# Kernel optimization log

Hardware: AMD Instinct MI355X
Metric: run time of the kernel (lower is better)

Reference implementation:

```python
import jax, jax.numpy as jnp
import numpy as np

HIDDEN = 1024
HEADS = 16
HEAD_DIM = HIDDEN // HEADS


def setup_inputs() -> dict:
    key = jax.random.key(0)
    ks = jax.random.split(key, 8)
    B, S = 2, 2048
    scale = 1.0 / np.sqrt(HIDDEN)
    inp = {
        "hidden_states": jax.random.normal(ks[0], (B, S, HIDDEN), dtype=jnp.float32),
        "attention_mask": jnp.zeros((B, 1, 1, S), dtype=jnp.float32),
        "q_w": jax.random.normal(ks[1], (HIDDEN, HIDDEN), dtype=jnp.float32) * scale,
        "q_b": jnp.zeros((HIDDEN,), dtype=jnp.float32),
        "k_w": jax.random.normal(ks[2], (HIDDEN, HIDDEN), dtype=jnp.float32) * scale,
        "k_b": jnp.zeros((HIDDEN,), dtype=jnp.float32),
        "v_w": jax.random.normal(ks[3], (HIDDEN, HIDDEN), dtype=jnp.float32) * scale,
        "v_b": jnp.zeros((HIDDEN,), dtype=jnp.float32),
    }
    return inp


def _split_heads(x):
    # [B, S, H] -> [B, heads, S, head_dim]
    B, S, _ = x.shape
    return x.reshape(B, S, HEADS, HEAD_DIM).transpose(0, 2, 1, 3)


def reference(hidden_states, attention_mask, q_w, q_b, k_w, k_b, v_w, v_b):
    # Linear projections (torch Linear: x @ W.T + b; here weights stored as [in, out])
    q = _split_heads(hidden_states @ q_w + q_b)  # [B, h, S, d]
    k = _split_heads(hidden_states @ k_w + k_b)
    v = _split_heads(hidden_states @ v_w + v_b)

    scores = jnp.einsum("bhqd,bhkd->bhqk", q, k) / jnp.sqrt(jnp.float32(HEAD_DIM))
    scores = scores + attention_mask  # additive mask, broadcast [B,1,1,S]
    probs = jax.nn.softmax(scores, axis=-1)
    # dropout prob = 0.0 -> identity
    ctx = jnp.einsum("bhqk,bhkd->bhqd", probs, v)  # [B, h, S, d]
    B, _, S, _ = ctx.shape
    ctx = ctx.transpose(0, 2, 1, 3).reshape(B, S, HIDDEN)
    return ctx
```

## Files before the change

kernel.cpp:

```cpp
#include <hip/hip_runtime.h>

typedef __bf16 bf16;
typedef __attribute__((ext_vector_type(8))) __bf16 bf16x8;
typedef __attribute__((ext_vector_type(4))) __bf16 bf16x4;
typedef __attribute__((ext_vector_type(4))) float f32x4;

#define MFMA(a, b, c) __builtin_amdgcn_mfma_f32_16x16x32_bf16((a), (b), (c), 0, 0, 0)
#define LOG2E 1.44269504088896340736f

__device__ __forceinline__ bf16x8 cvt8(float4 a, float4 b) {
  bf16x8 r;
  r[0] = (bf16)a.x; r[1] = (bf16)a.y; r[2] = (bf16)a.z; r[3] = (bf16)a.w;
  r[4] = (bf16)b.x; r[5] = (bf16)b.y; r[6] = (bf16)b.z; r[7] = (bf16)b.w;
  return r;
}

__device__ __forceinline__ void stage16(const bf16* g, bf16* l) {
  __builtin_amdgcn_global_load_lds(
      (const __attribute__((address_space(1))) void*)g,
      (__attribute__((address_space(3))) void*)l, 16, 0, 0);
}

__global__ __launch_bounds__(256)
void cvt(const float* __restrict__ hs, const float* __restrict__ qw,
         const float* __restrict__ kw, const float* __restrict__ vw,
         bf16* __restrict__ Xb, bf16* __restrict__ Wt) {
  const int bid = blockIdx.x, tid = threadIdx.x;
  if (bid < 2048) {
    size_t off = (size_t)bid * 2048 + tid * 8;
    float4 x0 = *(const float4*)(hs + off);
    float4 x1 = *(const float4*)(hs + off + 4);
    *(bf16x8*)(Xb + off) = cvt8(x0, x1);
  } else {
    int t = bid - 2048;
    int z = t >> 8, ti = t & 255;
    const float* W = (z == 0) ? qw : (z == 1) ? kw : vw;
    int k0 = (ti >> 4) * 64, n0 = (ti & 15) * 64;
    __shared__ bf16 T[64 * 72];
    #pragma unroll
    for (int i = 0; i < 16; ++i) {
      int e = i * 256 + tid;
      int kr = e >> 6, nc = e & 63;
      T[nc * 72 + kr] = (bf16)W[(size_t)(k0 + kr) * 1024 + n0 + nc];
    }
    __syncthreads();
    #pragma unroll
    for (int i = 0; i < 2; ++i) {
      int e = i * 256 + tid;
      int nr = e >> 3, kg = e & 7;
      *(bf16x8*)(Wt + (size_t)z * 1048576 + (size_t)(n0 + nr) * 1024 + k0 + kg * 8) =
          *(const bf16x8*)&T[nr * 72 + kg * 8];
    }
  }
}

__global__ __launch_bounds__(256, 3)
void qkv_gemm(const bf16* __restrict__ Xb, const bf16* __restrict__ Wt,
              const float* __restrict__ qbias, const float* __restrict__ kbias,
              const float* __restrict__ vbias,
              bf16* __restrict__ qo, bf16* __restrict__ ko, bf16* __restrict__ vo) {
  const int blk = blockIdx.x;
  const int xcd = blk & 7, slot = blk >> 3;
  const int mb = xcd * 4 + slot / 24;
  const int nb = slot % 24;
  const int z = nb >> 3, nbm = nb & 7;
  const bf16* W = Wt + (size_t)z * 1048576;

  const int tid = threadIdx.x;
  const int wave = tid >> 6, lane = tid & 63, quad = lane >> 4, c = lane & 15;
  const int wr = wave >> 1, wc = wave & 1;
  const int lrow = lane >> 3;
  const int lg = (lane & 7) ^ lrow;

  __shared__ bf16 As[128 * 64];
  __shared__ bf16 Bs[128 * 64];

  f32x4 acc[4][4] = {};

  for (int k0 = 0; k0 < 1024; k0 += 64) {
    #pragma unroll
    for (int i = 0; i < 4; ++i) {
      int r = wave * 32 + i * 8;
      stage16(Xb + (size_t)(mb * 128 + r + lrow) * 1024 + k0 + lg * 8, &As[r * 64]);
      stage16(W + (size_t)(nbm * 128 + r + lrow) * 1024 + k0 + lg * 8, &Bs[r * 64]);
    }
    __syncthreads();
    #pragma unroll
    for (int ch = 0; ch < 2; ++ch) {
      bf16x8 af[4];
      #pragma unroll
      for (int rt = 0; rt < 4; ++rt) {
        int row = wr * 64 + rt * 16 + c;
        af[rt] = *(const bf16x8*)&As[row * 64 + ((((ch << 2) | quad) ^ (c & 7)) << 3)];
      }
      #pragma unroll
      for (int nt = 0; nt < 4; ++nt) {
        int row = wc * 64 + nt * 16 + c;
        bf16x8 bfrag = *(const bf16x8*)&Bs[row * 64 + ((((ch << 2) | quad) ^ (c & 7)) << 3)];
        #pragma unroll
        for (int rt = 0; rt < 4; ++rt)
          acc[rt][nt] = MFMA(af[rt], bfrag, acc[rt][nt]);
      }
    }
    __syncthreads();
  }

  const float* bias = (z == 0) ? qbias : (z == 1) ? kbias : vbias;
  float bv[4];
  #pragma unroll
  for (int nt = 0; nt < 4; ++nt)
    bv[nt] = bias[nbm * 128 + wc * 64 + nt * 16 + c];

  if (z == 2) {
    #pragma unroll
    for (int rt = 0; rt < 4; ++rt)
      #pragma unroll
      for (int nt = 0; nt < 4; ++nt) {
        int m0 = mb * 128 + wr * 64 + rt * 16 + 4 * quad;
        int n = nbm * 128 + wc * 64 + nt * 16 + c;
        bf16x4 pk;
        #pragma unroll
        for (int reg = 0; reg < 4; ++reg) pk[reg] = (bf16)(acc[rt][nt][reg] + bv[nt]);
        int b = m0 >> 11, s0 = m0 & 2047, h = n >> 6, d = n & 63;
        *(bf16x4*)&vo[(((size_t)b * 16 + h) * 64 + d) * 2048 + s0] = pk;
      }
  } else {
    bf16* dst = (z == 0) ? qo : ko;
    const float scale = (z == 0) ? 0.125f * LOG2E : 1.0f;
    #pragma unroll
    for (int rt = 0; rt < 4; ++rt)
      #pragma unroll
      for (int nt = 0; nt < 4; ++nt)
        #pragma unroll
        for (int reg = 0; reg < 4; ++reg) {
          float v = (acc[rt][nt][reg] + bv[nt]) * scale;
          int m = mb * 128 + wr * 64 + rt * 16 + 4 * quad + reg;
          int n = nbm * 128 + wc * 64 + nt * 16 + c;
          int b = m >> 11, s = m & 2047, h = n >> 6, d = n & 63;
          dst[(((size_t)b * 16 + h) * 2048 + s) * 64 + d] = (bf16)v;
        }
  }
}

__global__ __launch_bounds__(512, 4)
void attn(const bf16* __restrict__ qg, const bf16* __restrict__ kg,
          const bf16* __restrict__ vtg, const float* __restrict__ mask,
          float* __restrict__ out) {
  const int blk = blockIdx.x;
  const int xcd = blk & 7, slot = blk >> 3;
  const int bh = xcd * 4 + (slot >> 4);
  const int qblk = slot & 15;
  const int b = bh >> 4, h = bh & 15;
  const int tid = threadIdx.x;
  const int wave = tid >> 6, lane = tid & 63, quad = lane >> 4, c = lane & 15;
  const int lrow = lane >> 3, lg = (lane & 7) ^ lrow;

  __shared__ bf16 Ks[64 * 64];
  __shared__ bf16 Vs[64 * 64];
  __shared__ bf16 Ps[8][1024];

  const bf16* qb_ = qg + (size_t)bh * 2048 * 64;
  const bf16* kb_ = kg + (size_t)bh * 2048 * 64;
  const bf16* vb_ = vtg + (size_t)bh * 64 * 2048;

  bf16x8 qf[2];
  #pragma unroll
  for (int ch = 0; ch < 2; ++ch)
    qf[ch] = *(const bf16x8*)(qb_ +
        (size_t)(qblk * 128 + wave * 16 + c) * 64 + ch * 32 + quad * 8);

  f32x4 o[4] = {};
  float lsum[4] = {};

  for (int kt = 0; kt < 32; ++kt) {
    {
      int r = wave * 8;
      stage16(kb_ + (size_t)(kt * 64 + r + lrow) * 64 + lg * 8, &Ks[r * 64]);
      stage16(vb_ + (size_t)(r + lrow) * 2048 + kt * 64 + lg * 8, &Vs[r * 64]);
    }
    __syncthreads();

    f32x4 s[4] = {};
    #pragma unroll
    for (int nt = 0; nt < 4; ++nt)
      #pragma unroll
      for (int ch = 0; ch < 2; ++ch) {
        bf16x8 kf = *(const bf16x8*)&Ks[(nt * 16 + c) * 64 +
                                        ((((ch << 2) | quad) ^ (c & 7)) << 3)];
        s[nt] = MFMA(qf[ch], kf, s[nt]);
      }

    float mv[4];
    #pragma unroll
    for (int nt = 0; nt < 4; ++nt)
      mv[nt] = mask[b * 2048 + kt * 64 + nt * 16 + c] * LOG2E;

    #pragma unroll
    for (int nt = 0; nt < 4; ++nt)
      #pragma unroll
      for (int reg = 0; reg < 4; ++reg) {
        float p = __builtin_amdgcn_exp2f(s[nt][reg] + mv[nt]);
        lsum[reg] += p;
        int r = 4 * quad + reg;
        int gk = nt * 2 + (c >> 3);
        Ps[wave][r * 64 + ((gk ^ (r & 7)) << 3) + (c & 7)] = (bf16)p;
      }
    __asm__ volatile("s_waitcnt lgkmcnt(0)" ::: "memory");

    #pragma unroll
    for (int ch = 0; ch < 2; ++ch) {
      bf16x8 pa = *(const bf16x8*)&Ps[wave][c * 64 +
                                           ((((ch << 2) | quad) ^ (c & 7)) << 3)];
      #pragma unroll
      for (int nt = 0; nt < 4; ++nt) {
        bf16x8 vf = *(const bf16x8*)&Vs[(nt * 16 + c) * 64 +
                                        ((((ch << 2) | quad) ^ (c & 7)) << 3)];
        o[nt] = MFMA(pa, vf, o[nt]);
      }
    }
    __syncthreads();
  }

  #pragma unroll
  for (int reg = 0; reg < 4; ++reg) {
    float l = lsum[reg];
    #pragma unroll
    for (int off = 1; off < 16; off <<= 1) l += __shfl_xor(l, off, 64);
    float inv = 1.0f / l;
    int srow = qblk * 128 + wave * 16 + 4 * quad + reg;
    #pragma unroll
    for (int nt = 0; nt < 4; ++nt)
      out[((size_t)b * 2048 + srow) * 1024 + h * 64 + nt * 16 + c] =
          o[nt][reg] * inv;
  }
}

extern "C" void kernel_launch(void* const* d_in, const int* in_sizes, int n_in,
                              void* d_out, int out_size, void* d_ws, size_t ws_size,
                              hipStream_t stream) {
  const float* hs   = (const float*)d_in[0];
  const float* mask = (const float*)d_in[1];
  const float* qw   = (const float*)d_in[2];
  const float* qb   = (const float*)d_in[3];
  const float* kw   = (const float*)d_in[4];
  const float* kb   = (const float*)d_in[5];
  const float* vw   = (const float*)d_in[6];
  const float* vb   = (const float*)d_in[7];
  float* out = (float*)d_out;

  bf16* Xb   = (bf16*)d_ws;
  bf16* Wt   = Xb + (size_t)4096 * 1024;
  bf16* q_ws = Wt + (size_t)3 * 1048576;
  bf16* k_ws = q_ws + (size_t)4096 * 1024;
  bf16* v_ws = k_ws + (size_t)4096 * 1024;

  cvt<<<dim3(2816), 256, 0, stream>>>(hs, qw, kw, vw, Xb, Wt);
  qkv_gemm<<<dim3(768), 256, 0, stream>>>(Xb, Wt, qb, kb, vb, q_ws, k_ws, v_ws);
  attn<<<dim3(512), 512, 0, stream>>>(q_ws, k_ws, v_ws, mask, out);
}
```

Baseline: 178.6 us.

## Double-buffer K/V tiles, keep P in registers via bpermute, shrink GEMM K-step

The attention kernel now double-buffers the K and V tiles in LDS, prefetching tile kt+1 while computing tile kt, so one barrier per iteration replaces two. It computes S transposed (K as the A operand) and redistributes the packed bf16 probabilities across lanes with ds_bpermute instead of writing them to and reading them from a per-wave LDS buffer. The row sum becomes one scalar per lane, reduced with fewer shuffles. The QKV GEMM switches to a 32-wide K step with precomputed addresses and a 4-way swizzle, halving LDS use, and the attention kernel drops its occupancy hint. Risks are more barriers in the GEMM, since it now has twice as many K iterations, and the cost of the permutes.

```diff
diff --git a/kernel.cpp b/kernel.cpp
--- a/kernel.cpp
+++ b/kernel.cpp
@@ -3,6 +3,7 @@
 typedef __bf16 bf16;
 typedef __attribute__((ext_vector_type(8))) __bf16 bf16x8;
 typedef __attribute__((ext_vector_type(4))) __bf16 bf16x4;
+typedef __attribute__((ext_vector_type(2))) __bf16 bf16x2;
 typedef __attribute__((ext_vector_type(4))) float f32x4;
 
 #define MFMA(a, b, c) __builtin_amdgcn_mfma_f32_16x16x32_bf16((a), (b), (c), 0, 0, 0)
@@ -13,6 +14,12 @@
   r[0] = (bf16)a.x; r[1] = (bf16)a.y; r[2] = (bf16)a.z; r[3] = (bf16)a.w;
   r[4] = (bf16)b.x; r[5] = (bf16)b.y; r[6] = (bf16)b.z; r[7] = (bf16)b.w;
   return r;
+}
+
+__device__ __forceinline__ int pk2(float x, float y) {
+  union { bf16x2 h; int i; } u;
+  u.h[0] = (bf16)x; u.h[1] = (bf16)y;
+  return u.i;
 }
 
 __device__ __forceinline__ void stage16(const bf16* g, bf16* l) {
@@ -69,38 +76,45 @@
   const int tid = threadIdx.x;
   const int wave = tid >> 6, lane = tid & 63, quad = lane >> 4, c = lane & 15;
   const int wr = wave >> 1, wc = wave & 1;
-  const int lrow = lane >> 3;
-  const int lg = (lane & 7) ^ lrow;
-
-  __shared__ bf16 As[128 * 64];
-  __shared__ bf16 Bs[128 * 64];
+  const int r4 = lane >> 2;
+  const int g4 = (lane & 3) ^ (r4 & 3);
+
+  __shared__ bf16 As[128 * 32];
+  __shared__ bf16 Bs[128 * 32];
+
+  const bf16* aS0 = Xb + (size_t)(mb * 128 + wave * 16 + r4) * 1024 + g4 * 8;
+  const bf16* aS1 = aS0 + (size_t)64 * 1024;
+  const bf16* bS0 = W + (size_t)(nbm * 128 + wave * 16 + r4) * 1024 + g4 * 8;
+  const bf16* bS1 = bS0 + (size_t)64 * 1024;
+  bf16* aD0 = &As[(wave * 16) * 32];
+  bf16* aD1 = &As[(64 + wave * 16) * 32];
+  bf16* bD0 = &Bs[(wave * 16) * 32];
+  bf16* bD1 = &Bs[(64 + wave * 16) * 32];
+
+  int aOff[4], bOff[4];
+  #pragma unroll
+  for (int t = 0; t < 4; ++t) {
+    aOff[t] = (wr * 64 + t * 16 + c) * 32 + ((quad ^ (c & 3)) << 3);
+    bOff[t] = (wc * 64 + t * 16 + c) * 32 + ((quad ^ (c & 3)) << 3);
+  }
 
   f32x4 acc[4][4] = {};
 
-  for (int k0 = 0; k0 < 1024; k0 += 64) {
-    #pragma unroll
-    for (int i = 0; i < 4; ++i) {
-      int r = wave * 32 + i * 8;
-      stage16(Xb + (size_t)(mb * 128 + r + lrow) * 1024 + k0 + lg * 8, &As[r * 64]);
-      stage16(W + (size_t)(nbm * 128 + r + lrow) * 1024 + k0 + lg * 8, &Bs[r * 64]);
-    }
-    __syncthreads();
-    #pragma unroll
-    for (int ch = 0; ch < 2; ++ch) {
-      bf16x8 af[4];
-      #pragma unroll
-      for (int rt = 0; rt < 4; ++rt) {
-        int row = wr * 64 + rt * 16 + c;
-        af[rt] = *(const bf16x8*)&As[row * 64 + ((((ch << 2) | quad) ^ (c & 7)) << 3)];
-      }
-      #pragma unroll
-      for (int nt = 0; nt < 4; ++nt) {
-        int row = wc * 64 + nt * 16 + c;
-        bf16x8 bfrag = *(const bf16x8*)&Bs[row * 64 + ((((ch << 2) | quad) ^ (c & 7)) << 3)];
-        #pragma unroll
-        for (int rt = 0; rt < 4; ++rt)
-          acc[rt][nt] = MFMA(af[rt], bfrag, acc[rt][nt]);
-      }
+  for (int k0 = 0; k0 < 1024; k0 += 32) {
+    stage16(aS0 + k0, aD0);
+    stage16(aS1 + k0, aD1);
+    stage16(bS0 + k0, bD0);
+    stage16(bS1 + k0, bD1);
+    __syncthreads();
+    bf16x8 af[4];
+    #pragma unroll
+    for (int rt = 0; rt < 4; ++rt) af[rt] = *(const bf16x8*)&As[aOff[rt]];
+    #pragma unroll
+    for (int nt = 0; nt < 4; ++nt) {
+      bf16x8 bfrag = *(const bf16x8*)&Bs[bOff[nt]];
+      #pragma unroll
+      for (int rt = 0; rt < 4; ++rt)
+        acc[rt][nt] = MFMA(af[rt], bfrag, acc[rt][nt]);
     }
     __syncthreads();
   }
@@ -142,7 +156,7 @@
   }
 }
 
-__global__ __launch_bounds__(512, 4)
+__global__ __launch_bounds__(512)
 void attn(const bf16* __restrict__ qg, const bf16* __restrict__ kg,
           const bf16* __restrict__ vtg, const float* __restrict__ mask,
           float* __restrict__ out) {
@@ -155,13 +169,13 @@
   const int wave = tid >> 6, lane = tid & 63, quad = lane >> 4, c = lane & 15;
   const int lrow = lane >> 3, lg = (lane & 7) ^ lrow;
 
-  __shared__ bf16 Ks[64 * 64];
-  __shared__ bf16 Vs[64 * 64];
-  __shared__ bf16 Ps[8][1024];
+  __shared__ bf16 Ks[2][64 * 64];
+  __shared__ bf16 Vs[2][64 * 64];
 
   const bf16* qb_ = qg + (size_t)bh * 2048 * 64;
   const bf16* kb_ = kg + (size_t)bh * 2048 * 64;
   const bf16* vb_ = vtg + (size_t)bh * 64 * 2048;
+  const float* mk_ = mask + (size_t)b * 2048;
 
   bf16x8 qf[2];
   #pragma unroll
@@ -169,64 +183,86 @@
     qf[ch] = *(const bf16x8*)(qb_ +
         (size_t)(qblk * 128 + wave * 16 + c) * 64 + ch * 32 + quad * 8);
 
+  const int idx0 = ((2 * (quad & 1) + (quad >> 1)) * 16 + c) << 2;
+  const int idx1 = idx0 ^ 64;
+  const bool qhi = (quad >= 2);
+  const bool qodd = (quad & 1);
+
   f32x4 o[4] = {};
-  float lsum[4] = {};
+  float lsum = 0.f;
+
+  {
+    int r = wave * 8;
+    stage16(kb_ + (size_t)(r + lrow) * 64 + lg * 8, &Ks[0][r * 64]);
+    stage16(vb_ + (size_t)(r + lrow) * 2048 + lg * 8, &Vs[0][r * 64]);
+  }
 
   for (int kt = 0; kt < 32; ++kt) {
-    {
+    __syncthreads();
+    const int cur = kt & 1;
+    if (kt < 31) {
       int r = wave * 8;
-      stage16(kb_ + (size_t)(kt * 64 + r + lrow) * 64 + lg * 8, &Ks[r * 64]);
-      stage16(vb_ + (size_t)(r + lrow) * 2048 + kt * 64 + lg * 8, &Vs[r * 64]);
-    }
-    __syncthreads();
+      stage16(kb_ + (size_t)((kt + 1) * 64 + r + lrow) * 64 + lg * 8,
+              &Ks[cur ^ 1][r * 64]);
+      stage16(vb_ + (size_t)(r + lrow) * 2048 + (kt + 1) * 64 + lg * 8,
+              &Vs[cur ^ 1][r * 64]);
+    }
 
     f32x4 s[4] = {};
     #pragma unroll
     for (int nt = 0; nt < 4; ++nt)
       #pragma unroll
       for (int ch = 0; ch < 2; ++ch) {
-        bf16x8 kf = *(const bf16x8*)&Ks[(nt * 16 + c) * 64 +
-                                        ((((ch << 2) | quad) ^ (c & 7)) << 3)];
-        s[nt] = MFMA(qf[ch], kf, s[nt]);
-      }
-
-    float mv[4];
-    #pragma unroll
-    for (int nt = 0; nt < 4; ++nt)
-      mv[nt] = mask[b * 2048 + kt * 64 + nt * 16 + c] * LOG2E;
-
-    #pragma unroll
-    for (int nt = 0; nt < 4; ++nt)
+        bf16x8 kf = *(const bf16x8*)&Ks[cur][(nt * 16 + c) * 64 +
+                                            ((((ch << 2) | quad) ^ (c & 7)) << 3)];
+        s[nt] = MFMA(kf, qf[ch], s[nt]);
+      }
+
+    int pk[4][2];
+    #pragma unroll
+    for (int nt = 0; nt < 4; ++nt) {
+      float4 mv = *(const float4*)&mk_[kt * 64 + nt * 16 + 4 * quad];
+      float mvf[4] = {mv.x, mv.y, mv.z, mv.w};
+      float p[4];
       #pragma unroll
       for (int reg = 0; reg < 4; ++reg) {
-        float p = __builtin_amdgcn_exp2f(s[nt][reg] + mv[nt]);
-        lsum[reg] += p;
-        int r = 4 * quad + reg;
-        int gk = nt * 2 + (c >> 3);
-        Ps[wave][r * 64 + ((gk ^ (r & 7)) << 3) + (c & 7)] = (bf16)p;
-      }
-    __asm__ volatile("s_waitcnt lgkmcnt(0)" ::: "memory");
+        p[reg] = __builtin_amdgcn_exp2f(fmaf(mvf[reg], LOG2E, s[nt][reg]));
+        lsum += p[reg];
+      }
+      pk[nt][0] = pk2(p[0], p[1]);
+      pk[nt][1] = pk2(p[2], p[3]);
+    }
 
     #pragma unroll
     for (int ch = 0; ch < 2; ++ch) {
-      bf16x8 pa = *(const bf16x8*)&Ps[wave][c * 64 +
-                                           ((((ch << 2) | quad) ^ (c & 7)) << 3)];
+      const int tA = 2 * ch, tB = 2 * ch + 1;
+      int sA0 = qodd ? pk[tB][0] : pk[tA][0];
+      int sA1 = qodd ? pk[tB][1] : pk[tA][1];
+      int sB0 = qodd ? pk[tA][0] : pk[tB][0];
+      int sB1 = qodd ? pk[tA][1] : pk[tB][1];
+      int rA0 = __builtin_amdgcn_ds_bpermute(idx0, sA0);
+      int rA1 = __builtin_amdgcn_ds_bpermute(idx0, sA1);
+      int rB0 = __builtin_amdgcn_ds_bpermute(idx1, sB0);
+      int rB1 = __builtin_amdgcn_ds_bpermute(idx1, sB1);
+      union { int i[4]; bf16x8 v; } pa;
+      pa.i[0] = qhi ? rB0 : rA0;
+      pa.i[1] = qhi ? rB1 : rA1;
+      pa.i[2] = qhi ? rA0 : rB0;
+      pa.i[3] = qhi ? rA1 : rB1;
       #pragma unroll
       for (int nt = 0; nt < 4; ++nt) {
-        bf16x8 vf = *(const bf16x8*)&Vs[(nt * 16 + c) * 64 +
-                                        ((((ch << 2) | quad) ^ (c & 7)) << 3)];
-        o[nt] = MFMA(pa, vf, o[nt]);
-      }
-    }
-    __syncthreads();
-  }
-
+        bf16x8 vf = *(const bf16x8*)&Vs[cur][(nt * 16 + c) * 64 +
+                                            ((((ch << 2) | quad) ^ (c & 7)) << 3)];
+        o[nt] = MFMA(pa.v, vf, o[nt]);
+      }
+    }
+  }
+
+  lsum += __shfl_xor(lsum, 16, 64);
+  lsum += __shfl_xor(lsum, 32, 64);
   #pragma unroll
   for (int reg = 0; reg < 4; ++reg) {
-    float l = lsum[reg];
-    #pragma unroll
-    for (int off = 1; off < 16; off <<= 1) l += __shfl_xor(l, off, 64);
-    float inv = 1.0f / l;
+    float inv = 1.0f / __shfl(lsum, 4 * quad + reg, 64);
     int srow = qblk * 128 + wave * 16 + 4 * quad + reg;
     #pragma unroll
     for (int nt = 0; nt < 4; ++nt)
```

Result: slower. 196.0 us (+9.8%).

## Halve GEMM K-tile and shrink attention blocks to 64 query rows

Applied to the files above, without the earlier changes.

The QKV GEMM now stages 32-wide K slices instead of 64, using a 4-way XOR swizzle and precomputed LDS offsets, which halves shared memory per block so more blocks can be resident. The attention kernel goes from 512-thread blocks covering 128 queries to 256-thread blocks covering 64 queries, doubling the grid to 1024 blocks. Each block now issues twice the K/V stage loads per wave. The aim is better occupancy and load balance, at the cost of twice as many barrier/sync iterations in the GEMM and twice the total K/V traffic in attention.

```diff
diff --git a/kernel.cpp b/kernel.cpp
--- a/kernel.cpp
+++ b/kernel.cpp
@@ -69,38 +69,45 @@
   const int tid = threadIdx.x;
   const int wave = tid >> 6, lane = tid & 63, quad = lane >> 4, c = lane & 15;
   const int wr = wave >> 1, wc = wave & 1;
-  const int lrow = lane >> 3;
-  const int lg = (lane & 7) ^ lrow;
-
-  __shared__ bf16 As[128 * 64];
-  __shared__ bf16 Bs[128 * 64];
+  const int r4 = lane >> 2;
+  const int g4 = (lane & 3) ^ (r4 & 3);
+
+  __shared__ bf16 As[128 * 32];
+  __shared__ bf16 Bs[128 * 32];
+
+  const bf16* aS0 = Xb + (size_t)(mb * 128 + wave * 16 + r4) * 1024 + g4 * 8;
+  const bf16* aS1 = aS0 + (size_t)64 * 1024;
+  const bf16* bS0 = W + (size_t)(nbm * 128 + wave * 16 + r4) * 1024 + g4 * 8;
+  const bf16* bS1 = bS0 + (size_t)64 * 1024;
+  bf16* aD0 = &As[(wave * 16) * 32];
+  bf16* aD1 = &As[(64 + wave * 16) * 32];
+  bf16* bD0 = &Bs[(wave * 16) * 32];
+  bf16* bD1 = &Bs[(64 + wave * 16) * 32];
+
+  int aOff[4], bOff[4];
+  #pragma unroll
+  for (int t = 0; t < 4; ++t) {
+    aOff[t] = (wr * 64 + t * 16 + c) * 32 + ((quad ^ (c & 3)) << 3);
+    bOff[t] = (wc * 64 + t * 16 + c) * 32 + ((quad ^ (c & 3)) << 3);
+  }
 
   f32x4 acc[4][4] = {};
 
-  for (int k0 = 0; k0 < 1024; k0 += 64) {
-    #pragma unroll
-    for (int i = 0; i < 4; ++i) {
-      int r = wave * 32 + i * 8;
-      stage16(Xb + (size_t)(mb * 128 + r + lrow) * 1024 + k0 + lg * 8, &As[r * 64]);
-      stage16(W + (size_t)(nbm * 128 + r + lrow) * 1024 + k0 + lg * 8, &Bs[r * 64]);
-    }
-    __syncthreads();
-    #pragma unroll
-    for (int ch = 0; ch < 2; ++ch) {
-      bf16x8 af[4];
-      #pragma unroll
-      for (int rt = 0; rt < 4; ++rt) {
-        int row = wr * 64 + rt * 16 + c;
-        af[rt] = *(const bf16x8*)&As[row * 64 + ((((ch << 2) | quad) ^ (c & 7)) << 3)];
-      }
-      #pragma unroll
-      for (int nt = 0; nt < 4; ++nt) {
-        int row = wc * 64 + nt * 16 + c;
-        bf16x8 bfrag = *(const bf16x8*)&Bs[row * 64 + ((((ch << 2) | quad) ^ (c & 7)) << 3)];
-        #pragma unroll
-        for (int rt = 0; rt < 4; ++rt)
-          acc[rt][nt] = MFMA(af[rt], bfrag, acc[rt][nt]);
-      }
+  for (int k0 = 0; k0 < 1024; k0 += 32) {
+    stage16(aS0 + k0, aD0);
+    stage16(aS1 + k0, aD1);
+    stage16(bS0 + k0, bD0);
+    stage16(bS1 + k0, bD1);
+    __syncthreads();
+    bf16x8 af[4];
+    #pragma unroll
+    for (int rt = 0; rt < 4; ++rt) af[rt] = *(const bf16x8*)&As[aOff[rt]];
+    #pragma unroll
+    for (int nt = 0; nt < 4; ++nt) {
+      bf16x8 bfrag = *(const bf16x8*)&Bs[bOff[nt]];
+      #pragma unroll
+      for (int rt = 0; rt < 4; ++rt)
+        acc[rt][nt] = MFMA(af[rt], bfrag, acc[rt][nt]);
     }
     __syncthreads();
   }
@@ -142,14 +149,14 @@
   }
 }
 
-__global__ __launch_bounds__(512, 4)
+__global__ __launch_bounds__(256, 4)
 void attn(const bf16* __restrict__ qg, const bf16* __restrict__ kg,
           const bf16* __restrict__ vtg, const float* __restrict__ mask,
           float* __restrict__ out) {
   const int blk = blockIdx.x;
   const int xcd = blk & 7, slot = blk >> 3;
-  const int bh = xcd * 4 + (slot >> 4);
-  const int qblk = slot & 15;
+  const int bh = xcd * 4 + (slot >> 5);
+  const int qblk = slot & 31;
   const int b = bh >> 4, h = bh & 15;
   const int tid = threadIdx.x;
   const int wave = tid >> 6, lane = tid & 63, quad = lane >> 4, c = lane & 15;
@@ -157,7 +164,7 @@
 
   __shared__ bf16 Ks[64 * 64];
   __shared__ bf16 Vs[64 * 64];
-  __shared__ bf16 Ps[8][1024];
+  __shared__ bf16 Ps[4][1024];
 
   const bf16* qb_ = qg + (size_t)bh * 2048 * 64;
   const bf16* kb_ = kg + (size_t)bh * 2048 * 64;
@@ -167,14 +174,15 @@
   #pragma unroll
   for (int ch = 0; ch < 2; ++ch)
     qf[ch] = *(const bf16x8*)(qb_ +
-        (size_t)(qblk * 128 + wave * 16 + c) * 64 + ch * 32 + quad * 8);
+        (size_t)(qblk * 64 + wave * 16 + c) * 64 + ch * 32 + quad * 8);
 
   f32x4 o[4] = {};
   float lsum[4] = {};
 
   for (int kt = 0; kt < 32; ++kt) {
-    {
-      int r = wave * 8;
+    #pragma unroll
+    for (int i = 0; i < 2; ++i) {
+      int r = wave * 16 + i * 8;
       stage16(kb_ + (size_t)(kt * 64 + r + lrow) * 64 + lg * 8, &Ks[r * 64]);
       stage16(vb_ + (size_t)(r + lrow) * 2048 + kt * 64 + lg * 8, &Vs[r * 64]);
     }
@@ -227,7 +235,7 @@
     #pragma unroll
     for (int off = 1; off < 16; off <<= 1) l += __shfl_xor(l, off, 64);
     float inv = 1.0f / l;
-    int srow = qblk * 128 + wave * 16 + 4 * quad + reg;
+    int srow = qblk * 64 + wave * 16 + 4 * quad + reg;
     #pragma unroll
     for (int nt = 0; nt < 4; ++nt)
       out[((size_t)b * 2048 + srow) * 1024 + h * 64 + nt * 16 + c] =
@@ -256,5 +264,5 @@
 
   cvt<<<dim3(2816), 256, 0, stream>>>(hs, qw, kw, vw, Xb, Wt);
   qkv_gemm<<<dim3(768), 256, 0, stream>>>(Xb, Wt, qb, kb, vb, q_ws, k_ws, v_ws);
-  attn<<<dim3(512), 512, 0, stream>>>(q_ws, k_ws, v_ws, mask, out);
-}
+  attn<<<dim3(1024), 256, 0, stream>>>(q_ws, k_ws, v_ws, mask, out);
+}
```

Result: no change. 180.4 us (+1.0%).
